# Kernel tuning notes

Hardware: AMD Instinct MI355X
Metric: run time of the kernel (lower is better)

The kernel has to match this reference:

```python
import jax, jax.numpy as jnp
import numpy as np

N_SRC = 100_000
N_DST = 100_000
N_EDGES = 1_600_000
D_IN = 256
N_HEADS = 4
OUT_FEATS = 32
NEG_SLOPE = 0.2


def setup_inputs() -> dict:
    key = jax.random.key(0)
    k1, k2, k3, k4, k5, k6, k7 = jax.random.split(key, 7)
    return {
        "feat_src": jax.random.normal(k1, (N_SRC, D_IN), dtype=jnp.float32),
        "feat_dst": jax.random.normal(k2, (N_DST, D_IN), dtype=jnp.float32),
        "w_src": jax.random.normal(k3, (D_IN, N_HEADS * OUT_FEATS), dtype=jnp.float32) * 0.05,
        "w_dst": jax.random.normal(k4, (D_IN, N_HEADS * OUT_FEATS), dtype=jnp.float32) * 0.05,
        "attn": jax.random.normal(k5, (N_HEADS, 2 * OUT_FEATS), dtype=jnp.float32) * 0.05,
        "src_idx": jax.random.randint(k6, (N_EDGES,), 0, N_SRC, dtype=jnp.int32),
        "dst_idx": jax.random.randint(k7, (N_EDGES,), 0, N_DST, dtype=jnp.int32),
    }


def reference(feat_src, feat_dst, w_src, w_dst, attn, src_idx, dst_idx):
    H, two_d = attn.shape
    D = two_d // 2
    n_dst = feat_dst.shape[0]
    # node transformations (dropout rate = 0.0 -> identity)
    fs = (feat_src @ w_src).reshape(-1, H, D)   # [Ns, H, D]
    fd = (feat_dst @ w_dst).reshape(-1, H, D)   # [Nd, H, D]
    # per-node attention logits: e_dst uses first half, e_src second half
    e_dst = (fd * attn[:, :D]).sum(-1)          # [Nd, H]
    e_src = (fs * attn[:, D:]).sum(-1)          # [Ns, H]
    # u_add_v on edges + leaky relu
    e = e_src[src_idx] + e_dst[dst_idx]         # [E, H]
    e = jnp.where(e > 0, e, NEG_SLOPE * e)
    # edge softmax: segment softmax over incoming edges of each dst node
    m = jax.ops.segment_max(e, dst_idx, num_segments=n_dst)       # [Nd, H]
    m = jnp.where(jnp.isfinite(m), m, 0.0)                        # empty segments
    ex = jnp.exp(e - m[dst_idx])                                  # [E, H]
    denom = jax.ops.segment_sum(ex, dst_idx, num_segments=n_dst)  # [Nd, H]
    a = ex / denom[dst_idx]                                       # [E, H]
    # u_mul_e + sum aggregation
    msg = fs[src_idx] * a[:, :, None]                             # [E, H, D]
    out = jax.ops.segment_sum(msg, dst_idx, num_segments=n_dst)   # [Nd, H, D]
    return jax.nn.relu(out.reshape(n_dst, H * D))
```

## Files before the change

kernel.cpp:

```cpp
#include <hip/hip_runtime.h>

#define N_NODES 100000
#define N_EDGES 1600000
#define D_IN    256
#define HD      128
#define NEG_SLOPE 0.2f

#define BUK_SH    5
#define BUK_NODES 32
#define NBUCKETS ((N_NODES + BUK_NODES - 1) / BUK_NODES)
#define BUK_CAP  1024
#define BUK_CH   8192
#define NB_BUK   ((N_EDGES + BUK_CH - 1) / BUK_CH)

#define NB_GEMM ((N_NODES + 255) / 256)
#define NB_EDST ((N_NODES + 15) / 16)
#define NB_MEGA (NB_GEMM + NB_BUK + NB_EDST)
#define NB_ZERO ((NBUCKETS + 255) / 256)

typedef __bf16 bf16x8 __attribute__((ext_vector_type(8)));
typedef float  f32x4  __attribute__((ext_vector_type(4)));

__device__ __forceinline__ float lrelu_exp(float v) {
  v = v > 0.f ? v : NEG_SLOPE * v;
  return __expf(v);
}
__device__ __forceinline__ float bf_lo(unsigned u) { return __uint_as_float(u << 16); }
__device__ __forceinline__ float bf_hi(unsigned u) { return __uint_as_float(u & 0xffff0000u); }

__global__ __launch_bounds__(256) void prep_kernel(const float* __restrict__ w_src,
                                                   const float* __restrict__ w_dst,
                                                   const float* __restrict__ attn,
                                                   ushort* __restrict__ wT,
                                                   float* __restrict__ v_dst,
                                                   int* __restrict__ bcur) {
  int bid = blockIdx.x;
  int tid = threadIdx.x;
  if (bid < 128) {
    int idx = bid * 256 + tid;
    int k = idx >> 7, n = idx & 127;
    __bf16 bv = (__bf16)w_src[idx];
    wT[n * 256 + k] = *(const ushort*)&bv;
  } else if (bid == 128) {
    int k = tid;
    for (int h = 0; h < 4; ++h) {
      float s = 0.f;
      for (int d = 0; d < 32; ++d)
        s += w_dst[k * HD + h * 32 + d] * attn[h * 64 + d];
      v_dst[k * 4 + h] = s;
    }
  } else {
    int i = (bid - 129) * 256 + tid;
    if (i < NBUCKETS) bcur[i] = 0;
  }
}

__global__ __launch_bounds__(1024) void mega_kernel(const float* __restrict__ A,
                                                    const ushort* __restrict__ wT16,
                                                    const float* __restrict__ attn,
                                                    unsigned* __restrict__ fs16,
                                                    float* __restrict__ e_src,
                                                    const int* __restrict__ src,
                                                    const int* __restrict__ dstv,
                                                    int* __restrict__ bcur,
                                                    unsigned* __restrict__ ebuk,
                                                    const float* __restrict__ feat_dst,
                                                    const float* __restrict__ v_dst,
                                                    float* __restrict__ e_dst,
                                                    int M) {
  __shared__ ushort Bl[128 * 256];
  __shared__ int bh[NBUCKETS];
  const int bid = blockIdx.x;
  const int tid = threadIdx.x;
  const int lane = tid & 63, wid = tid >> 6;
  const int lr = lane & 15, hi = lane >> 4;

  if (bid < NB_GEMM) {
    {
      const uint4* wg4 = (const uint4*)wT16;
#pragma unroll
      for (int i = 0; i < 4; ++i) {
        int c = i * 1024 + tid;
        int col = c >> 5;
        unsigned byte = ((unsigned)c * 16u) ^ (((unsigned)col & 31u) << 4);
        *(uint4*)((char*)Bl + byte) = wg4[c];
      }
    }

    f32x4 acc[8];
    const f32x4 zf = {0.f, 0.f, 0.f, 0.f};
#pragma unroll
    for (int n = 0; n < 8; ++n) acc[n] = zf;

    const int bm = bid * 256;
    int row0 = bm + wid * 16 + lr;
    int row0c = row0 < M ? row0 : M - 1;
    const float* a0p = A + (size_t)row0c * D_IN;

    __syncthreads();

#pragma unroll
    for (int ks = 0; ks < 8; ++ks) {
      const int ko = ks * 32 + hi * 8;
      float4 u0 = *(const float4*)(a0p + ko);
      float4 u1 = *(const float4*)(a0p + ko + 4);
      bf16x8 af0;
      af0[0] = (__bf16)u0.x; af0[1] = (__bf16)u0.y; af0[2] = (__bf16)u0.z; af0[3] = (__bf16)u0.w;
      af0[4] = (__bf16)u1.x; af0[5] = (__bf16)u1.y; af0[6] = (__bf16)u1.z; af0[7] = (__bf16)u1.w;
      bf16x8 bf[8];
#pragma unroll
      for (int n = 0; n < 8; ++n) {
        unsigned col = (unsigned)(n * 16 + lr);
        unsigned byte = (col * 512u + (unsigned)(ks * 64 + hi * 16)) ^ ((col & 31u) << 4);
        bf[n] = *(const bf16x8*)((const char*)Bl + byte);
      }
#pragma unroll
      for (int n = 0; n < 8; ++n)
        acc[n] = __builtin_amdgcn_mfma_f32_16x16x32_bf16(af0, bf[n], acc[n], 0, 0, 0);
    }

#pragma unroll
    for (int n = 0; n < 8; ++n) {
#pragma unroll
      for (int r4 = 0; r4 < 4; ++r4) {
        float val = acc[n][r4];
        float pv  = __shfl_xor(val, 1, 64);
        int gr = bm + wid * 16 + hi * 4 + r4;
        if (!(lane & 1) && gr < M) {
          __bf16 b0 = (__bf16)val, b1 = (__bf16)pv;
          unsigned pk = ((unsigned)*(const ushort*)&b1 << 16) | *(const ushort*)&b0;
          fs16[(size_t)gr * 64 + n * 8 + (lr >> 1)] = pk;
        }
      }
    }

#pragma unroll
    for (int gh = 0; gh < 4; ++gh) {
      float av0 = attn[gh * 64 + 32 + lr];
      float av1 = attn[gh * 64 + 48 + lr];
#pragma unroll
      for (int r4 = 0; r4 < 4; ++r4) {
        float s = acc[2 * gh][r4] * av0 + acc[2 * gh + 1][r4] * av1;
        s += __shfl_xor(s, 1, 64);
        s += __shfl_xor(s, 2, 64);
        s += __shfl_xor(s, 4, 64);
        s += __shfl_xor(s, 8, 64);
        int gr = bm + wid * 16 + hi * 4 + r4;
        if (lr == 0 && gr < M) e_src[(size_t)gr * 4 + gh] = s;
      }
    }
  } else if (bid < NB_GEMM + NB_BUK) {
    const int e0 = (bid - NB_GEMM) * BUK_CH;
    for (int j = tid; j < NBUCKETS; j += 1024) bh[j] = 0;
    __syncthreads();
    for (int i = tid; i < BUK_CH; i += 1024) {
      int e = e0 + i;
      if (e < N_EDGES) atomicAdd(&bh[dstv[e] >> BUK_SH], 1);
    }
    __syncthreads();
    for (int j = tid; j < NBUCKETS; j += 1024) {
      int c = bh[j];
      bh[j] = (c > 0) ? atomicAdd(&bcur[j], c) : 0;
    }
    __syncthreads();
    for (int i = tid; i < BUK_CH; i += 1024) {
      int e = e0 + i;
      if (e < N_EDGES) {
        int d = dstv[e];
        int b = d >> BUK_SH;
        int p = atomicAdd(&bh[b], 1);
        if (p < BUK_CAP)
          ebuk[(size_t)b * BUK_CAP + p] =
              ((unsigned)src[e] << BUK_SH) | (unsigned)(d & (BUK_NODES - 1));
      }
    }
  } else {
    int gw = (bid - NB_GEMM - NB_BUK) * 16 + wid;
    if (gw < N_NODES) {
      float4 f = *(const float4*)(feat_dst + (size_t)gw * D_IN + lane * 4);
      float acc0 = 0.f, acc1 = 0.f, acc2 = 0.f, acc3 = 0.f;
      const float* fp = &f.x;
#pragma unroll
      for (int j = 0; j < 4; ++j) {
        float fv = fp[j];
        float4 vv = *(const float4*)(v_dst + (size_t)(lane * 4 + j) * 4);
        acc0 = fmaf(fv, vv.x, acc0);
        acc1 = fmaf(fv, vv.y, acc1);
        acc2 = fmaf(fv, vv.z, acc2);
        acc3 = fmaf(fv, vv.w, acc3);
      }
#pragma unroll
      for (int off = 1; off < 64; off <<= 1) {
        acc0 += __shfl_xor(acc0, off, 64);
        acc1 += __shfl_xor(acc1, off, 64);
        acc2 += __shfl_xor(acc2, off, 64);
        acc3 += __shfl_xor(acc3, off, 64);
      }
      if (lane == 0) *(float4*)(e_dst + (size_t)gw * 4) = make_float4(acc0, acc1, acc2, acc3);
    }
  }
}

__global__ __launch_bounds__(256) void agg_kernel(const unsigned* __restrict__ ebuk,
                                                  const int* __restrict__ bcur,
                                                  const float4* __restrict__ e_src,
                                                  const float4* __restrict__ e_dst,
                                                  const unsigned* __restrict__ fs16,
                                                  float* __restrict__ out, int N) {
  __shared__ unsigned sorted_e[BUK_CAP];
  __shared__ int lcnt[BUK_NODES];
  __shared__ int lofs_s[BUK_NODES + 1];
  __shared__ int lcur[BUK_NODES];
  __shared__ float sh_ex[4][4][72];
  const int tid = threadIdx.x;
  const int wslot = tid >> 6;
  const int lane = tid & 63;
  const int lo = blockIdx.x * BUK_NODES;
  const size_t start = (size_t)blockIdx.x * BUK_CAP;
  const int cnt_e = min(bcur[blockIdx.x], BUK_CAP);

  if (tid < BUK_NODES) lcnt[tid] = 0;
  __syncthreads();
  for (int i = tid; i < cnt_e; i += 256)
    atomicAdd(&lcnt[ebuk[start + i] & (BUK_NODES - 1)], 1);
  __syncthreads();
  if (tid == 0) {
    int run = 0;
    for (int j = 0; j < BUK_NODES; ++j) {
      lofs_s[j] = run; lcur[j] = run; run += lcnt[j];
    }
    lofs_s[BUK_NODES] = run;
  }
  __syncthreads();
  for (int i = tid; i < cnt_e; i += 256) {
    unsigned e = ebuk[start + i];
    int p = atomicAdd(&lcur[e & (BUK_NODES - 1)], 1);
    sorted_e[p] = e;
  }
  __syncthreads();

  const int g = lane >> 4;
  const int q = lane & 15;
  const int h = q >> 2;

  for (int nl = wslot * 8; nl < wslot * 8 + 8; ++nl) {
    int node = lo + nl;
    if (node >= N) break;
    const int nb = lofs_s[nl], ne = lofs_s[nl + 1];
    const float4 ed = e_dst[node];
    float a0=0.f,a1=0.f,a2=0.f,a3=0.f,a4=0.f,a5=0.f,a6=0.f,a7=0.f,den=0.f;

    for (int cb = nb; cb < ne; cb += 64) {
      int cs = min(64, ne - cb);
      if (lane < cs) {
        unsigned ent = sorted_e[cb + lane];
        int s = (int)(ent >> BUK_SH);
        float4 a = e_src[s];
        sh_ex[wslot][0][lane] = lrelu_exp(a.x + ed.x);
        sh_ex[wslot][1][lane] = lrelu_exp(a.y + ed.y);
        sh_ex[wslot][2][lane] = lrelu_exp(a.z + ed.z);
        sh_ex[wslot][3][lane] = lrelu_exp(a.w + ed.w);
      }
      __threadfence_block();
      int j = 0;
      for (; j + 4 <= cs; j += 4) {
        int e = j + g;
        int s = (int)(sorted_e[cb + e] >> BUK_SH);
        float ex = sh_ex[wslot][h][e];
        uint4 u = *(const uint4*)(fs16 + (size_t)s * 64 + q * 4);
        a0 = fmaf(ex, bf_lo(u.x), a0); a1 = fmaf(ex, bf_hi(u.x), a1);
        a2 = fmaf(ex, bf_lo(u.y), a2); a3 = fmaf(ex, bf_hi(u.y), a3);
        a4 = fmaf(ex, bf_lo(u.z), a4); a5 = fmaf(ex, bf_hi(u.z), a5);
        a6 = fmaf(ex, bf_lo(u.w), a6); a7 = fmaf(ex, bf_hi(u.w), a7);
        den += ex;
      }
      if (j < cs) {
        int e = j + g;
        bool pred = e < cs;
        int ec = pred ? e : 0;
        int s = (int)(sorted_e[cb + ec] >> BUK_SH);
        float ex = pred ? sh_ex[wslot][h][ec] : 0.f;
        uint4 u = *(const uint4*)(fs16 + (size_t)s * 64 + q * 4);
        a0 = fmaf(ex, bf_lo(u.x), a0); a1 = fmaf(ex, bf_hi(u.x), a1);
        a2 = fmaf(ex, bf_lo(u.y), a2); a3 = fmaf(ex, bf_hi(u.y), a3);
        a4 = fmaf(ex, bf_lo(u.z), a4); a5 = fmaf(ex, bf_hi(u.z), a5);
        a6 = fmaf(ex, bf_lo(u.w), a6); a7 = fmaf(ex, bf_hi(u.w), a7);
        den += ex;
      }
      __threadfence_block();
    }

    den += __shfl_xor(den, 16, 64); den += __shfl_xor(den, 32, 64);
    a0 += __shfl_xor(a0, 16, 64); a0 += __shfl_xor(a0, 32, 64);
    a1 += __shfl_xor(a1, 16, 64); a1 += __shfl_xor(a1, 32, 64);
    a2 += __shfl_xor(a2, 16, 64); a2 += __shfl_xor(a2, 32, 64);
    a3 += __shfl_xor(a3, 16, 64); a3 += __shfl_xor(a3, 32, 64);
    a4 += __shfl_xor(a4, 16, 64); a4 += __shfl_xor(a4, 32, 64);
    a5 += __shfl_xor(a5, 16, 64); a5 += __shfl_xor(a5, 32, 64);
    a6 += __shfl_xor(a6, 16, 64); a6 += __shfl_xor(a6, 32, 64);
    a7 += __shfl_xor(a7, 16, 64); a7 += __shfl_xor(a7, 32, 64);
    if (lane < 16) {
      float inv = den > 0.f ? 1.f / den : 0.f;
      float4 o1, o2;
      o1.x = fmaxf(a0 * inv, 0.f); o1.y = fmaxf(a1 * inv, 0.f);
      o1.z = fmaxf(a2 * inv, 0.f); o1.w = fmaxf(a3 * inv, 0.f);
      o2.x = fmaxf(a4 * inv, 0.f); o2.y = fmaxf(a5 * inv, 0.f);
      o2.z = fmaxf(a6 * inv, 0.f); o2.w = fmaxf(a7 * inv, 0.f);
      float* op = out + (size_t)node * HD + q * 8;
      *(float4*)(op)     = o1;
      *(float4*)(op + 4) = o2;
    }
  }
}

extern "C" void kernel_launch(void* const* d_in, const int* in_sizes, int n_in,
                              void* d_out, int out_size, void* d_ws, size_t ws_size,
                              hipStream_t stream) {
  const float* feat_src = (const float*)d_in[0];
  const float* feat_dst = (const float*)d_in[1];
  const float* w_src    = (const float*)d_in[2];
  const float* w_dst    = (const float*)d_in[3];
  const float* attn     = (const float*)d_in[4];
  const int*   src_idx  = (const int*)d_in[5];
  const int*   dst_idx  = (const int*)d_in[6];
  float* out = (float*)d_out;
  char* ws = (char*)d_ws;

  unsigned* fs16  = (unsigned*)(ws);
  float*    e_src = (float*)(ws + 25600000);
  float*    e_dst = (float*)(ws + 27200000);
  unsigned* ebuk  = (unsigned*)(ws + 28800000);
  float*    v_dst = (float*)(ws + 41600000);
  ushort*   wT16  = (ushort*)(ws + 41604096);
  int*      bcur  = (int*)  (ws + 41669632);

  prep_kernel<<<129 + NB_ZERO, 256, 0, stream>>>(w_src, w_dst, attn, wT16, v_dst, bcur);

  mega_kernel<<<NB_MEGA, 1024, 0, stream>>>(feat_src, wT16, attn, fs16, e_src,
                                            src_idx, dst_idx, bcur, ebuk,
                                            feat_dst, v_dst, e_dst, N_NODES);

  agg_kernel<<<NBUCKETS, 256, 0, stream>>>(ebuk, bcur,
      (const float4*)e_src, (const float4*)e_dst, fs16, out, N_NODES);
}
```

Measured before the change: 178.9 us.

## Make mega and agg kernels persistent with fewer, larger per-block work chunks

The GEMM blocks now process two 256-row tiles each, so the staged weight tile in LDS is reused. The bucketing blocks take larger edge chunks, and the e_dst blocks loop over a contiguous node range with software-prefetched rows and v_dst hoisted into registers. The aggregation kernel becomes grid-stride over buckets with a fixed 1024-block grid. This cuts block launch and setup overhead and LDS reloads, at the cost of less parallelism and possible load imbalance across blocks.

```diff
diff --git a/kernel.cpp b/kernel.cpp
--- a/kernel.cpp
+++ b/kernel.cpp
@@ -10,13 +10,16 @@
 #define BUK_NODES 32
 #define NBUCKETS ((N_NODES + BUK_NODES - 1) / BUK_NODES)
 #define BUK_CAP  1024
-#define BUK_CH   8192
+#define BUK_CH   25000
 #define NB_BUK   ((N_EDGES + BUK_CH - 1) / BUK_CH)
 
-#define NB_GEMM ((N_NODES + 255) / 256)
-#define NB_EDST ((N_NODES + 15) / 16)
-#define NB_MEGA (NB_GEMM + NB_BUK + NB_EDST)
+#define NB_GEMM_T ((N_NODES + 255) / 256)
+#define NB_GEMM   ((NB_GEMM_T + 1) / 2)
+#define NB_EDST   192
+#define EDST_CH   ((N_NODES + NB_EDST - 1) / NB_EDST)
+#define NB_MEGA   (NB_GEMM + NB_BUK + NB_EDST)
 #define NB_ZERO ((NBUCKETS + 255) / 256)
+#define NB_AGG  1024
 
 typedef __bf16 bf16x8 __attribute__((ext_vector_type(8)));
 typedef float  f32x4  __attribute__((ext_vector_type(4)));
@@ -86,67 +89,71 @@
         *(uint4*)((char*)Bl + byte) = wg4[c];
       }
     }
-
-    f32x4 acc[8];
-    const f32x4 zf = {0.f, 0.f, 0.f, 0.f};
-#pragma unroll
-    for (int n = 0; n < 8; ++n) acc[n] = zf;
-
-    const int bm = bid * 256;
-    int row0 = bm + wid * 16 + lr;
-    int row0c = row0 < M ? row0 : M - 1;
-    const float* a0p = A + (size_t)row0c * D_IN;
-
-    __syncthreads();
-
-#pragma unroll
-    for (int ks = 0; ks < 8; ++ks) {
-      const int ko = ks * 32 + hi * 8;
-      float4 u0 = *(const float4*)(a0p + ko);
-      float4 u1 = *(const float4*)(a0p + ko + 4);
-      bf16x8 af0;
-      af0[0] = (__bf16)u0.x; af0[1] = (__bf16)u0.y; af0[2] = (__bf16)u0.z; af0[3] = (__bf16)u0.w;
-      af0[4] = (__bf16)u1.x; af0[5] = (__bf16)u1.y; af0[6] = (__bf16)u1.z; af0[7] = (__bf16)u1.w;
-      bf16x8 bf[8];
+    __syncthreads();
+
+    const int t0 = bid * 2;
+    const int t1 = min(t0 + 2, NB_GEMM_T);
+    for (int t = t0; t < t1; ++t) {
+      const int bm = t * 256;
+
+      f32x4 acc[8];
+      const f32x4 zf = {0.f, 0.f, 0.f, 0.f};
+#pragma unroll
+      for (int n = 0; n < 8; ++n) acc[n] = zf;
+
+      int row0 = bm + wid * 16 + lr;
+      int row0c = row0 < M ? row0 : M - 1;
+      const float* a0p = A + (size_t)row0c * D_IN;
+
+#pragma unroll
+      for (int ks = 0; ks < 8; ++ks) {
+        const int ko = ks * 32 + hi * 8;
+        float4 u0 = *(const float4*)(a0p + ko);
+        float4 u1 = *(const float4*)(a0p + ko + 4);
+        bf16x8 af0;
+        af0[0] = (__bf16)u0.x; af0[1] = (__bf16)u0.y; af0[2] = (__bf16)u0.z; af0[3] = (__bf16)u0.w;
+        af0[4] = (__bf16)u1.x; af0[5] = (__bf16)u1.y; af0[6] = (__bf16)u1.z; af0[7] = (__bf16)u1.w;
+        bf16x8 bf[8];
+#pragma unroll
+        for (int n = 0; n < 8; ++n) {
+          unsigned col = (unsigned)(n * 16 + lr);
+          unsigned byte = (col * 512u + (unsigned)(ks * 64 + hi * 16)) ^ ((col & 31u) << 4);
+          bf[n] = *(const bf16x8*)((const char*)Bl + byte);
+        }
+#pragma unroll
+        for (int n = 0; n < 8; ++n)
+          acc[n] = __builtin_amdgcn_mfma_f32_16x16x32_bf16(af0, bf[n], acc[n], 0, 0, 0);
+      }
+
 #pragma unroll
       for (int n = 0; n < 8; ++n) {
-        unsigned col = (unsigned)(n * 16 + lr);
-        unsigned byte = (col * 512u + (unsigned)(ks * 64 + hi * 16)) ^ ((col & 31u) << 4);
-        bf[n] = *(const bf16x8*)((const char*)Bl + byte);
-      }
-#pragma unroll
-      for (int n = 0; n < 8; ++n)
-        acc[n] = __builtin_amdgcn_mfma_f32_16x16x32_bf16(af0, bf[n], acc[n], 0, 0, 0);
-    }
-
-#pragma unroll
-    for (int n = 0; n < 8; ++n) {
-#pragma unroll
-      for (int r4 = 0; r4 < 4; ++r4) {
-        float val = acc[n][r4];
-        float pv  = __shfl_xor(val, 1, 64);
-        int gr = bm + wid * 16 + hi * 4 + r4;
-        if (!(lane & 1) && gr < M) {
-          __bf16 b0 = (__bf16)val, b1 = (__bf16)pv;
-          unsigned pk = ((unsigned)*(const ushort*)&b1 << 16) | *(const ushort*)&b0;
-          fs16[(size_t)gr * 64 + n * 8 + (lr >> 1)] = pk;
-        }
-      }
-    }
-
-#pragma unroll
-    for (int gh = 0; gh < 4; ++gh) {
-      float av0 = attn[gh * 64 + 32 + lr];
-      float av1 = attn[gh * 64 + 48 + lr];
-#pragma unroll
-      for (int r4 = 0; r4 < 4; ++r4) {
-        float s = acc[2 * gh][r4] * av0 + acc[2 * gh + 1][r4] * av1;
-        s += __shfl_xor(s, 1, 64);
-        s += __shfl_xor(s, 2, 64);
-        s += __shfl_xor(s, 4, 64);
-        s += __shfl_xor(s, 8, 64);
-        int gr = bm + wid * 16 + hi * 4 + r4;
-        if (lr == 0 && gr < M) e_src[(size_t)gr * 4 + gh] = s;
+#pragma unroll
+        for (int r4 = 0; r4 < 4; ++r4) {
+          float val = acc[n][r4];
+          float pv  = __shfl_xor(val, 1, 64);
+          int gr = bm + wid * 16 + hi * 4 + r4;
+          if (!(lane & 1) && gr < M) {
+            __bf16 b0 = (__bf16)val, b1 = (__bf16)pv;
+            unsigned pk = ((unsigned)*(const ushort*)&b1 << 16) | *(const ushort*)&b0;
+            fs16[(size_t)gr * 64 + n * 8 + (lr >> 1)] = pk;
+          }
+        }
+      }
+
+#pragma unroll
+      for (int gh = 0; gh < 4; ++gh) {
+        float av0 = attn[gh * 64 + 32 + lr];
+        float av1 = attn[gh * 64 + 48 + lr];
+#pragma unroll
+        for (int r4 = 0; r4 < 4; ++r4) {
+          float s = acc[2 * gh][r4] * av0 + acc[2 * gh + 1][r4] * av1;
+          s += __shfl_xor(s, 1, 64);
+          s += __shfl_xor(s, 2, 64);
+          s += __shfl_xor(s, 4, 64);
+          s += __shfl_xor(s, 8, 64);
+          int gr = bm + wid * 16 + hi * 4 + r4;
+          if (lr == 0 && gr < M) e_src[(size_t)gr * 4 + gh] = s;
+        }
       }
     }
   } else if (bid < NB_GEMM + NB_BUK) {
@@ -175,28 +182,36 @@
       }
     }
   } else {
-    int gw = (bid - NB_GEMM - NB_BUK) * 16 + wid;
-    if (gw < N_NODES) {
-      float4 f = *(const float4*)(feat_dst + (size_t)gw * D_IN + lane * 4);
-      float acc0 = 0.f, acc1 = 0.f, acc2 = 0.f, acc3 = 0.f;
-      const float* fp = &f.x;
-#pragma unroll
-      for (int j = 0; j < 4; ++j) {
-        float fv = fp[j];
-        float4 vv = *(const float4*)(v_dst + (size_t)(lane * 4 + j) * 4);
-        acc0 = fmaf(fv, vv.x, acc0);
-        acc1 = fmaf(fv, vv.y, acc1);
-        acc2 = fmaf(fv, vv.z, acc2);
-        acc3 = fmaf(fv, vv.w, acc3);
-      }
-#pragma unroll
-      for (int off = 1; off < 64; off <<= 1) {
-        acc0 += __shfl_xor(acc0, off, 64);
-        acc1 += __shfl_xor(acc1, off, 64);
-        acc2 += __shfl_xor(acc2, off, 64);
-        acc3 += __shfl_xor(acc3, off, 64);
-      }
-      if (lane == 0) *(float4*)(e_dst + (size_t)gw * 4) = make_float4(acc0, acc1, acc2, acc3);
+    const int rb = bid - NB_GEMM - NB_BUK;
+    const int b0 = rb * EDST_CH;
+    const int bend = min(b0 + EDST_CH, N_NODES);
+    float4 vv0 = *(const float4*)(v_dst + (size_t)(lane * 4 + 0) * 4);
+    float4 vv1 = *(const float4*)(v_dst + (size_t)(lane * 4 + 1) * 4);
+    float4 vv2 = *(const float4*)(v_dst + (size_t)(lane * 4 + 2) * 4);
+    float4 vv3 = *(const float4*)(v_dst + (size_t)(lane * 4 + 3) * 4);
+    int n = b0 + wid;
+    if (n < bend) {
+      float4 f = *(const float4*)(feat_dst + (size_t)n * D_IN + lane * 4);
+      for (;;) {
+        const int nn = n + 16;
+        float4 f2;
+        const bool more = nn < bend;
+        if (more) f2 = *(const float4*)(feat_dst + (size_t)nn * D_IN + lane * 4);
+        float acc0 = fmaf(f.x, vv0.x, fmaf(f.y, vv1.x, fmaf(f.z, vv2.x, f.w * vv3.x)));
+        float acc1 = fmaf(f.x, vv0.y, fmaf(f.y, vv1.y, fmaf(f.z, vv2.y, f.w * vv3.y)));
+        float acc2 = fmaf(f.x, vv0.z, fmaf(f.y, vv1.z, fmaf(f.z, vv2.z, f.w * vv3.z)));
+        float acc3 = fmaf(f.x, vv0.w, fmaf(f.y, vv1.w, fmaf(f.z, vv2.w, f.w * vv3.w)));
+#pragma unroll
+        for (int off = 1; off < 64; off <<= 1) {
+          acc0 += __shfl_xor(acc0, off, 64);
+          acc1 += __shfl_xor(acc1, off, 64);
+          acc2 += __shfl_xor(acc2, off, 64);
+          acc3 += __shfl_xor(acc3, off, 64);
+        }
+        if (lane == 0) *(float4*)(e_dst + (size_t)n * 4) = make_float4(acc0, acc1, acc2, acc3);
+        if (!more) break;
+        f = f2; n = nn;
+      }
     }
   }
 }
@@ -215,100 +230,104 @@
   const int tid = threadIdx.x;
   const int wslot = tid >> 6;
   const int lane = tid & 63;
-  const int lo = blockIdx.x * BUK_NODES;
-  const size_t start = (size_t)blockIdx.x * BUK_CAP;
-  const int cnt_e = min(bcur[blockIdx.x], BUK_CAP);
-
-  if (tid < BUK_NODES) lcnt[tid] = 0;
-  __syncthreads();
-  for (int i = tid; i < cnt_e; i += 256)
-    atomicAdd(&lcnt[ebuk[start + i] & (BUK_NODES - 1)], 1);
-  __syncthreads();
-  if (tid == 0) {
-    int run = 0;
-    for (int j = 0; j < BUK_NODES; ++j) {
-      lofs_s[j] = run; lcur[j] = run; run += lcnt[j];
-    }
-    lofs_s[BUK_NODES] = run;
-  }
-  __syncthreads();
-  for (int i = tid; i < cnt_e; i += 256) {
-    unsigned e = ebuk[start + i];
-    int p = atomicAdd(&lcur[e & (BUK_NODES - 1)], 1);
-    sorted_e[p] = e;
-  }
-  __syncthreads();
 
   const int g = lane >> 4;
   const int q = lane & 15;
   const int h = q >> 2;
 
-  for (int nl = wslot * 8; nl < wslot * 8 + 8; ++nl) {
-    int node = lo + nl;
-    if (node >= N) break;
-    const int nb = lofs_s[nl], ne = lofs_s[nl + 1];
-    const float4 ed = e_dst[node];
-    float a0=0.f,a1=0.f,a2=0.f,a3=0.f,a4=0.f,a5=0.f,a6=0.f,a7=0.f,den=0.f;
-
-    for (int cb = nb; cb < ne; cb += 64) {
-      int cs = min(64, ne - cb);
-      if (lane < cs) {
-        unsigned ent = sorted_e[cb + lane];
-        int s = (int)(ent >> BUK_SH);
-        float4 a = e_src[s];
-        sh_ex[wslot][0][lane] = lrelu_exp(a.x + ed.x);
-        sh_ex[wslot][1][lane] = lrelu_exp(a.y + ed.y);
-        sh_ex[wslot][2][lane] = lrelu_exp(a.z + ed.z);
-        sh_ex[wslot][3][lane] = lrelu_exp(a.w + ed.w);
-      }
-      __threadfence_block();
-      int j = 0;
-      for (; j + 4 <= cs; j += 4) {
-        int e = j + g;
-        int s = (int)(sorted_e[cb + e] >> BUK_SH);
-        float ex = sh_ex[wslot][h][e];
-        uint4 u = *(const uint4*)(fs16 + (size_t)s * 64 + q * 4);
-        a0 = fmaf(ex, bf_lo(u.x), a0); a1 = fmaf(ex, bf_hi(u.x), a1);
-        a2 = fmaf(ex, bf_lo(u.y), a2); a3 = fmaf(ex, bf_hi(u.y), a3);
-        a4 = fmaf(ex, bf_lo(u.z), a4); a5 = fmaf(ex, bf_hi(u.z), a5);
-        a6 = fmaf(ex, bf_lo(u.w), a6); a7 = fmaf(ex, bf_hi(u.w), a7);
-        den += ex;
-      }
-      if (j < cs) {
-        int e = j + g;
-        bool pred = e < cs;
-        int ec = pred ? e : 0;
-        int s = (int)(sorted_e[cb + ec] >> BUK_SH);
-        float ex = pred ? sh_ex[wslot][h][ec] : 0.f;
-        uint4 u = *(const uint4*)(fs16 + (size_t)s * 64 + q * 4);
-        a0 = fmaf(ex, bf_lo(u.x), a0); a1 = fmaf(ex, bf_hi(u.x), a1);
-        a2 = fmaf(ex, bf_lo(u.y), a2); a3 = fmaf(ex, bf_hi(u.y), a3);
-        a4 = fmaf(ex, bf_lo(u.z), a4); a5 = fmaf(ex, bf_hi(u.z), a5);
-        a6 = fmaf(ex, bf_lo(u.w), a6); a7 = fmaf(ex, bf_hi(u.w), a7);
-        den += ex;
-      }
-      __threadfence_block();
-    }
-
-    den += __shfl_xor(den, 16, 64); den += __shfl_xor(den, 32, 64);
-    a0 += __shfl_xor(a0, 16, 64); a0 += __shfl_xor(a0, 32, 64);
-    a1 += __shfl_xor(a1, 16, 64); a1 += __shfl_xor(a1, 32, 64);
-    a2 += __shfl_xor(a2, 16, 64); a2 += __shfl_xor(a2, 32, 64);
-    a3 += __shfl_xor(a3, 16, 64); a3 += __shfl_xor(a3, 32, 64);
-    a4 += __shfl_xor(a4, 16, 64); a4 += __shfl_xor(a4, 32, 64);
-    a5 += __shfl_xor(a5, 16, 64); a5 += __shfl_xor(a5, 32, 64);
-    a6 += __shfl_xor(a6, 16, 64); a6 += __shfl_xor(a6, 32, 64);
-    a7 += __shfl_xor(a7, 16, 64); a7 += __shfl_xor(a7, 32, 64);
-    if (lane < 16) {
-      float inv = den > 0.f ? 1.f / den : 0.f;
-      float4 o1, o2;
-      o1.x = fmaxf(a0 * inv, 0.f); o1.y = fmaxf(a1 * inv, 0.f);
-      o1.z = fmaxf(a2 * inv, 0.f); o1.w = fmaxf(a3 * inv, 0.f);
-      o2.x = fmaxf(a4 * inv, 0.f); o2.y = fmaxf(a5 * inv, 0.f);
-      o2.z = fmaxf(a6 * inv, 0.f); o2.w = fmaxf(a7 * inv, 0.f);
-      float* op = out + (size_t)node * HD + q * 8;
-      *(float4*)(op)     = o1;
-      *(float4*)(op + 4) = o2;
+  for (int bk = blockIdx.x; bk < NBUCKETS; bk += NB_AGG) {
+    __syncthreads();
+    const int lo = bk * BUK_NODES;
+    const size_t start = (size_t)bk * BUK_CAP;
+    const int cnt_e = min(bcur[bk], BUK_CAP);
+
+    if (tid < BUK_NODES) lcnt[tid] = 0;
+    __syncthreads();
+    for (int i = tid; i < cnt_e; i += 256)
+      atomicAdd(&lcnt[ebuk[start + i] & (BUK_NODES - 1)], 1);
+    __syncthreads();
+    if (tid == 0) {
+      int run = 0;
+      for (int j = 0; j < BUK_NODES; ++j) {
+        lofs_s[j] = run; lcur[j] = run; run += lcnt[j];
+      }
+      lofs_s[BUK_NODES] = run;
+    }
+    __syncthreads();
+    for (int i = tid; i < cnt_e; i += 256) {
+      unsigned e = ebuk[start + i];
+      int p = atomicAdd(&lcur[e & (BUK_NODES - 1)], 1);
+      sorted_e[p] = e;
+    }
+    __syncthreads();
+
+    for (int nl = wslot * 8; nl < wslot * 8 + 8; ++nl) {
+      int node = lo + nl;
+      if (node >= N) break;
+      const int nb = lofs_s[nl], ne = lofs_s[nl + 1];
+      const float4 ed = e_dst[node];
+      float a0=0.f,a1=0.f,a2=0.f,a3=0.f,a4=0.f,a5=0.f,a6=0.f,a7=0.f,den=0.f;
+
+      for (int cb = nb; cb < ne; cb += 64) {
+        int cs = min(64, ne - cb);
+        if (lane < cs) {
+          unsigned ent = sorted_e[cb + lane];
+          int s = (int)(ent >> BUK_SH);
+          float4 a = e_src[s];
+          sh_ex[wslot][0][lane] = lrelu_exp(a.x + ed.x);
+          sh_ex[wslot][1][lane] = lrelu_exp(a.y + ed.y);
+          sh_ex[wslot][2][lane] = lrelu_exp(a.z + ed.z);
+          sh_ex[wslot][3][lane] = lrelu_exp(a.w + ed.w);
+        }
+        __threadfence_block();
+        int j = 0;
+        for (; j + 4 <= cs; j += 4) {
+          int e = j + g;
+          int s = (int)(sorted_e[cb + e] >> BUK_SH);
+          float ex = sh_ex[wslot][h][e];
+          uint4 u = *(const uint4*)(fs16 + (size_t)s * 64 + q * 4);
+          a0 = fmaf(ex, bf_lo(u.x), a0); a1 = fmaf(ex, bf_hi(u.x), a1);
+          a2 = fmaf(ex, bf_lo(u.y), a2); a3 = fmaf(ex, bf_hi(u.y), a3);
+          a4 = fmaf(ex, bf_lo(u.z), a4); a5 = fmaf(ex, bf_hi(u.z), a5);
+          a6 = fmaf(ex, bf_lo(u.w), a6); a7 = fmaf(ex, bf_hi(u.w), a7);
+          den += ex;
+        }
+        if (j < cs) {
+          int e = j + g;
+          bool pred = e < cs;
+          int ec = pred ? e : 0;
+          int s = (int)(sorted_e[cb + ec] >> BUK_SH);
+          float ex = pred ? sh_ex[wslot][h][ec] : 0.f;
+          uint4 u = *(const uint4*)(fs16 + (size_t)s * 64 + q * 4);
+          a0 = fmaf(ex, bf_lo(u.x), a0); a1 = fmaf(ex, bf_hi(u.x), a1);
+          a2 = fmaf(ex, bf_lo(u.y), a2); a3 = fmaf(ex, bf_hi(u.y), a3);
+          a4 = fmaf(ex, bf_lo(u.z), a4); a5 = fmaf(ex, bf_hi(u.z), a5);
+          a6 = fmaf(ex, bf_lo(u.w), a6); a7 = fmaf(ex, bf_hi(u.w), a7);
+          den += ex;
+        }
+        __threadfence_block();
+      }
+
+      den += __shfl_xor(den, 16, 64); den += __shfl_xor(den, 32, 64);
+      a0 += __shfl_xor(a0, 16, 64); a0 += __shfl_xor(a0, 32, 64);
+      a1 += __shfl_xor(a1, 16, 64); a1 += __shfl_xor(a1, 32, 64);
+      a2 += __shfl_xor(a2, 16, 64); a2 += __shfl_xor(a2, 32, 64);
+      a3 += __shfl_xor(a3, 16, 64); a3 += __shfl_xor(a3, 32, 64);
+      a4 += __shfl_xor(a4, 16, 64); a4 += __shfl_xor(a4, 32, 64);
+      a5 += __shfl_xor(a5, 16, 64); a5 += __shfl_xor(a5, 32, 64);
+      a6 += __shfl_xor(a6, 16, 64); a6 += __shfl_xor(a6, 32, 64);
+      a7 += __shfl_xor(a7, 16, 64); a7 += __shfl_xor(a7, 32, 64);
+      if (lane < 16) {
+        float inv = den > 0.f ? 1.f / den : 0.f;
+        float4 o1, o2;
+        o1.x = fmaxf(a0 * inv, 0.f); o1.y = fmaxf(a1 * inv, 0.f);
+        o1.z = fmaxf(a2 * inv, 0.f); o1.w = fmaxf(a3 * inv, 0.f);
+        o2.x = fmaxf(a4 * inv, 0.f); o2.y = fmaxf(a5 * inv, 0.f);
+        o2.z = fmaxf(a6 * inv, 0.f); o2.w = fmaxf(a7 * inv, 0.f);
+        float* op = out + (size_t)node * HD + q * 8;
+        *(float4*)(op)     = o1;
+        *(float4*)(op + 4) = o2;
+      }
     }
   }
 }
@@ -340,6 +359,6 @@
                                             src_idx, dst_idx, bcur, ebuk,
                                             feat_dst, v_dst, e_dst, N_NODES);
 
-  agg_kernel<<<NBUCKETS, 256, 0, stream>>>(ebuk, bcur,
+  agg_kernel<<<NB_AGG, 256, 0, stream>>>(ebuk, bcur,
       (const float4*)e_src, (const float4*)e_dst, fs16, out, N_NODES);
 }
```

After: 317.0 us. 77.2% more time.

## Split fused mega kernel into separate GEMM, e_dst, and bucketing kernels

Applied to the files above, without the earlier changes.

Breaks the heterogeneous mega kernel into three launches: the bf16 MFMA GEMM, a grid-stride e_dst projection kernel with 256-thread blocks and v_dst cached in LDS, and the edge bucketing kernel. Each branch no longer pays for the union of LDS (64KB B tile plus bucket histogram) and register pressure of the others, which should let more blocks fit per CU. The e_dst kernel now uses 16 lanes per node instead of a full wave. The cost is that the three phases now run serially instead of overlapping, plus extra launch overhead.

```diff
diff --git a/kernel.cpp b/kernel.cpp
--- a/kernel.cpp
+++ b/kernel.cpp
@@ -14,8 +14,7 @@
 #define NB_BUK   ((N_EDGES + BUK_CH - 1) / BUK_CH)
 
 #define NB_GEMM ((N_NODES + 255) / 256)
-#define NB_EDST ((N_NODES + 15) / 16)
-#define NB_MEGA (NB_GEMM + NB_BUK + NB_EDST)
+#define NB_EDST 1024
 #define NB_ZERO ((NBUCKETS + 255) / 256)
 
 typedef __bf16 bf16x8 __attribute__((ext_vector_type(8)));
@@ -55,148 +54,154 @@
   }
 }
 
-__global__ __launch_bounds__(1024) void mega_kernel(const float* __restrict__ A,
+__global__ __launch_bounds__(1024) void gemm_kernel(const float* __restrict__ A,
                                                     const ushort* __restrict__ wT16,
                                                     const float* __restrict__ attn,
                                                     unsigned* __restrict__ fs16,
                                                     float* __restrict__ e_src,
-                                                    const int* __restrict__ src,
-                                                    const int* __restrict__ dstv,
-                                                    int* __restrict__ bcur,
-                                                    unsigned* __restrict__ ebuk,
-                                                    const float* __restrict__ feat_dst,
-                                                    const float* __restrict__ v_dst,
-                                                    float* __restrict__ e_dst,
                                                     int M) {
   __shared__ ushort Bl[128 * 256];
-  __shared__ int bh[NBUCKETS];
   const int bid = blockIdx.x;
   const int tid = threadIdx.x;
   const int lane = tid & 63, wid = tid >> 6;
   const int lr = lane & 15, hi = lane >> 4;
 
-  if (bid < NB_GEMM) {
-    {
-      const uint4* wg4 = (const uint4*)wT16;
-#pragma unroll
-      for (int i = 0; i < 4; ++i) {
-        int c = i * 1024 + tid;
-        int col = c >> 5;
-        unsigned byte = ((unsigned)c * 16u) ^ (((unsigned)col & 31u) << 4);
-        *(uint4*)((char*)Bl + byte) = wg4[c];
+  {
+    const uint4* wg4 = (const uint4*)wT16;
+#pragma unroll
+    for (int i = 0; i < 4; ++i) {
+      int c = i * 1024 + tid;
+      int col = c >> 5;
+      unsigned byte = ((unsigned)c * 16u) ^ (((unsigned)col & 31u) << 4);
+      *(uint4*)((char*)Bl + byte) = wg4[c];
+    }
+  }
+
+  f32x4 acc[8];
+  const f32x4 zf = {0.f, 0.f, 0.f, 0.f};
+#pragma unroll
+  for (int n = 0; n < 8; ++n) acc[n] = zf;
+
+  const int bm = bid * 256;
+  int row0 = bm + wid * 16 + lr;
+  int row0c = row0 < M ? row0 : M - 1;
+  const float* a0p = A + (size_t)row0c * D_IN;
+
+  __syncthreads();
+
+#pragma unroll
+  for (int ks = 0; ks < 8; ++ks) {
+    const int ko = ks * 32 + hi * 8;
+    float4 u0 = *(const float4*)(a0p + ko);
+    float4 u1 = *(const float4*)(a0p + ko + 4);
+    bf16x8 af0;
+    af0[0] = (__bf16)u0.x; af0[1] = (__bf16)u0.y; af0[2] = (__bf16)u0.z; af0[3] = (__bf16)u0.w;
+    af0[4] = (__bf16)u1.x; af0[5] = (__bf16)u1.y; af0[6] = (__bf16)u1.z; af0[7] = (__bf16)u1.w;
+    bf16x8 bf[8];
+#pragma unroll
+    for (int n = 0; n < 8; ++n) {
+      unsigned col = (unsigned)(n * 16 + lr);
+      unsigned byte = (col * 512u + (unsigned)(ks * 64 + hi * 16)) ^ ((col & 31u) << 4);
+      bf[n] = *(const bf16x8*)((const char*)Bl + byte);
+    }
+#pragma unroll
+    for (int n = 0; n < 8; ++n)
+      acc[n] = __builtin_amdgcn_mfma_f32_16x16x32_bf16(af0, bf[n], acc[n], 0, 0, 0);
+  }
+
+#pragma unroll
+  for (int n = 0; n < 8; ++n) {
+#pragma unroll
+    for (int r4 = 0; r4 < 4; ++r4) {
+      float val = acc[n][r4];
+      float pv  = __shfl_xor(val, 1, 64);
+      int gr = bm + wid * 16 + hi * 4 + r4;
+      if (!(lane & 1) && gr < M) {
+        __bf16 b0 = (__bf16)val, b1 = (__bf16)pv;
+        unsigned pk = ((unsigned)*(const ushort*)&b1 << 16) | *(const ushort*)&b0;
+        fs16[(size_t)gr * 64 + n * 8 + (lr >> 1)] = pk;
       }
     }
-
-    f32x4 acc[8];
-    const f32x4 zf = {0.f, 0.f, 0.f, 0.f};
-#pragma unroll
-    for (int n = 0; n < 8; ++n) acc[n] = zf;
-
-    const int bm = bid * 256;
-    int row0 = bm + wid * 16 + lr;
-    int row0c = row0 < M ? row0 : M - 1;
-    const float* a0p = A + (size_t)row0c * D_IN;
-
-    __syncthreads();
-
-#pragma unroll
-    for (int ks = 0; ks < 8; ++ks) {
-      const int ko = ks * 32 + hi * 8;
-      float4 u0 = *(const float4*)(a0p + ko);
-      float4 u1 = *(const float4*)(a0p + ko + 4);
-      bf16x8 af0;
-      af0[0] = (__bf16)u0.x; af0[1] = (__bf16)u0.y; af0[2] = (__bf16)u0.z; af0[3] = (__bf16)u0.w;
-      af0[4] = (__bf16)u1.x; af0[5] = (__bf16)u1.y; af0[6] = (__bf16)u1.z; af0[7] = (__bf16)u1.w;
-      bf16x8 bf[8];
-#pragma unroll
-      for (int n = 0; n < 8; ++n) {
-        unsigned col = (unsigned)(n * 16 + lr);
-        unsigned byte = (col * 512u + (unsigned)(ks * 64 + hi * 16)) ^ ((col & 31u) << 4);
-        bf[n] = *(const bf16x8*)((const char*)Bl + byte);
-      }
-#pragma unroll
-      for (int n = 0; n < 8; ++n)
-        acc[n] = __builtin_amdgcn_mfma_f32_16x16x32_bf16(af0, bf[n], acc[n], 0, 0, 0);
-    }
-
-#pragma unroll
-    for (int n = 0; n < 8; ++n) {
-#pragma unroll
-      for (int r4 = 0; r4 < 4; ++r4) {
-        float val = acc[n][r4];
-        float pv  = __shfl_xor(val, 1, 64);
-        int gr = bm + wid * 16 + hi * 4 + r4;
-        if (!(lane & 1) && gr < M) {
-          __bf16 b0 = (__bf16)val, b1 = (__bf16)pv;
-          unsigned pk = ((unsigned)*(const ushort*)&b1 << 16) | *(const ushort*)&b0;
-          fs16[(size_t)gr * 64 + n * 8 + (lr >> 1)] = pk;
-        }
-      }
-    }
-
-#pragma unroll
-    for (int gh = 0; gh < 4; ++gh) {
-      float av0 = attn[gh * 64 + 32 + lr];
-      float av1 = attn[gh * 64 + 48 + lr];
-#pragma unroll
-      for (int r4 = 0; r4 < 4; ++r4) {
-        float s = acc[2 * gh][r4] * av0 + acc[2 * gh + 1][r4] * av1;
-        s += __shfl_xor(s, 1, 64);
-        s += __shfl_xor(s, 2, 64);
-        s += __shfl_xor(s, 4, 64);
-        s += __shfl_xor(s, 8, 64);
-        int gr = bm + wid * 16 + hi * 4 + r4;
-        if (lr == 0 && gr < M) e_src[(size_t)gr * 4 + gh] = s;
-      }
-    }
-  } else if (bid < NB_GEMM + NB_BUK) {
-    const int e0 = (bid - NB_GEMM) * BUK_CH;
-    for (int j = tid; j < NBUCKETS; j += 1024) bh[j] = 0;
-    __syncthreads();
-    for (int i = tid; i < BUK_CH; i += 1024) {
-      int e = e0 + i;
-      if (e < N_EDGES) atomicAdd(&bh[dstv[e] >> BUK_SH], 1);
-    }
-    __syncthreads();
-    for (int j = tid; j < NBUCKETS; j += 1024) {
-      int c = bh[j];
-      bh[j] = (c > 0) ? atomicAdd(&bcur[j], c) : 0;
-    }
-    __syncthreads();
-    for (int i = tid; i < BUK_CH; i += 1024) {
-      int e = e0 + i;
-      if (e < N_EDGES) {
-        int d = dstv[e];
-        int b = d >> BUK_SH;
-        int p = atomicAdd(&bh[b], 1);
-        if (p < BUK_CAP)
-          ebuk[(size_t)b * BUK_CAP + p] =
-              ((unsigned)src[e] << BUK_SH) | (unsigned)(d & (BUK_NODES - 1));
-      }
-    }
-  } else {
-    int gw = (bid - NB_GEMM - NB_BUK) * 16 + wid;
-    if (gw < N_NODES) {
-      float4 f = *(const float4*)(feat_dst + (size_t)gw * D_IN + lane * 4);
-      float acc0 = 0.f, acc1 = 0.f, acc2 = 0.f, acc3 = 0.f;
-      const float* fp = &f.x;
-#pragma unroll
-      for (int j = 0; j < 4; ++j) {
-        float fv = fp[j];
-        float4 vv = *(const float4*)(v_dst + (size_t)(lane * 4 + j) * 4);
-        acc0 = fmaf(fv, vv.x, acc0);
-        acc1 = fmaf(fv, vv.y, acc1);
-        acc2 = fmaf(fv, vv.z, acc2);
-        acc3 = fmaf(fv, vv.w, acc3);
-      }
-#pragma unroll
-      for (int off = 1; off < 64; off <<= 1) {
-        acc0 += __shfl_xor(acc0, off, 64);
-        acc1 += __shfl_xor(acc1, off, 64);
-        acc2 += __shfl_xor(acc2, off, 64);
-        acc3 += __shfl_xor(acc3, off, 64);
-      }
-      if (lane == 0) *(float4*)(e_dst + (size_t)gw * 4) = make_float4(acc0, acc1, acc2, acc3);
+  }
+
+#pragma unroll
+  for (int gh = 0; gh < 4; ++gh) {
+    float av0 = attn[gh * 64 + 32 + lr];
+    float av1 = attn[gh * 64 + 48 + lr];
+#pragma unroll
+    for (int r4 = 0; r4 < 4; ++r4) {
+      float s = acc[2 * gh][r4] * av0 + acc[2 * gh + 1][r4] * av1;
+      s += __shfl_xor(s, 1, 64);
+      s += __shfl_xor(s, 2, 64);
+      s += __shfl_xor(s, 4, 64);
+      s += __shfl_xor(s, 8, 64);
+      int gr = bm + wid * 16 + hi * 4 + r4;
+      if (lr == 0 && gr < M) e_src[(size_t)gr * 4 + gh] = s;
+    }
+  }
+}
+
+__global__ __launch_bounds__(256) void edst_kernel(const float* __restrict__ feat_dst,
+                                                   const float* __restrict__ v_dst,
+                                                   float* __restrict__ e_dst) {
+  __shared__ float4 vds[256];
+  const int tid = threadIdx.x;
+  vds[tid] = ((const float4*)v_dst)[tid];
+  __syncthreads();
+  const int l = tid & 15;
+  const int grp = tid >> 4;
+  for (int n = blockIdx.x * 16 + grp; n < N_NODES; n += NB_EDST * 16) {
+    const float* fp = feat_dst + (size_t)n * D_IN;
+    float ax = 0.f, ay = 0.f, az = 0.f, aw = 0.f;
+#pragma unroll
+    for (int c = 0; c < 4; ++c) {
+      const int k0 = c * 64 + l * 4;
+      float4 f = *(const float4*)(fp + k0);
+      float4 v0 = vds[k0 + 0], v1 = vds[k0 + 1], v2 = vds[k0 + 2], v3 = vds[k0 + 3];
+      ax = fmaf(f.x, v0.x, fmaf(f.y, v1.x, fmaf(f.z, v2.x, fmaf(f.w, v3.x, ax))));
+      ay = fmaf(f.x, v0.y, fmaf(f.y, v1.y, fmaf(f.z, v2.y, fmaf(f.w, v3.y, ay))));
+      az = fmaf(f.x, v0.z, fmaf(f.y, v1.z, fmaf(f.z, v2.z, fmaf(f.w, v3.z, az))));
+      aw = fmaf(f.x, v0.w, fmaf(f.y, v1.w, fmaf(f.z, v2.w, fmaf(f.w, v3.w, aw))));
+    }
+#pragma unroll
+    for (int off = 1; off < 16; off <<= 1) {
+      ax += __shfl_xor(ax, off, 64);
+      ay += __shfl_xor(ay, off, 64);
+      az += __shfl_xor(az, off, 64);
+      aw += __shfl_xor(aw, off, 64);
+    }
+    if (l == 0) *(float4*)(e_dst + (size_t)n * 4) = make_float4(ax, ay, az, aw);
+  }
+}
+
+__global__ __launch_bounds__(1024) void bucket_kernel(const int* __restrict__ src,
+                                                      const int* __restrict__ dstv,
+                                                      int* __restrict__ bcur,
+                                                      unsigned* __restrict__ ebuk) {
+  __shared__ int bh[NBUCKETS];
+  const int tid = threadIdx.x;
+  const int e0 = blockIdx.x * BUK_CH;
+  for (int j = tid; j < NBUCKETS; j += 1024) bh[j] = 0;
+  __syncthreads();
+  for (int i = tid; i < BUK_CH; i += 1024) {
+    int e = e0 + i;
+    if (e < N_EDGES) atomicAdd(&bh[dstv[e] >> BUK_SH], 1);
+  }
+  __syncthreads();
+  for (int j = tid; j < NBUCKETS; j += 1024) {
+    int c = bh[j];
+    bh[j] = (c > 0) ? atomicAdd(&bcur[j], c) : 0;
+  }
+  __syncthreads();
+  for (int i = tid; i < BUK_CH; i += 1024) {
+    int e = e0 + i;
+    if (e < N_EDGES) {
+      int d = dstv[e];
+      int b = d >> BUK_SH;
+      int p = atomicAdd(&bh[b], 1);
+      if (p < BUK_CAP)
+        ebuk[(size_t)b * BUK_CAP + p] =
+            ((unsigned)src[e] << BUK_SH) | (unsigned)(d & (BUK_NODES - 1));
     }
   }
 }
@@ -336,9 +341,11 @@
 
   prep_kernel<<<129 + NB_ZERO, 256, 0, stream>>>(w_src, w_dst, attn, wT16, v_dst, bcur);
 
-  mega_kernel<<<NB_MEGA, 1024, 0, stream>>>(feat_src, wT16, attn, fs16, e_src,
-                                            src_idx, dst_idx, bcur, ebuk,
-                                            feat_dst, v_dst, e_dst, N_NODES);
+  gemm_kernel<<<NB_GEMM, 1024, 0, stream>>>(feat_src, wT16, attn, fs16, e_src, N_NODES);
+
+  edst_kernel<<<NB_EDST, 256, 0, stream>>>(feat_dst, v_dst, e_dst);
+
+  bucket_kernel<<<NB_BUK, 1024, 0, stream>>>(src_idx, dst_idx, bcur, ebuk);
 
   agg_kernel<<<NBUCKETS, 256, 0, stream>>>(ebuk, bcur,
       (const float4*)e_src, (const float4*)e_dst, fs16, out, N_NODES);
```

After: 178.6 us. Within noise of the previous version (-0.2%).
